# Kernel optimization log

Hardware: AMD Instinct MI355X
Metric: run time of the kernel (lower is better)

Reference implementation:

```python
import jax, jax.numpy as jnp
import numpy as np

N_NODES = 8192
N_FEAT = 256
N_EDGES = 131072
K = 4


def setup_inputs() -> dict:
    key = jax.random.key(0)
    k1, k2, k3 = jax.random.split(key, 3)
    x = jax.random.normal(k1, (N_NODES, N_FEAT), dtype=jnp.float32)
    edge_index = jax.random.randint(k2, (2, N_EDGES), 0, N_NODES, dtype=jnp.int64)
    edge_weight = jax.random.uniform(k3, (N_EDGES,), dtype=jnp.float32)
    return {"k": K, "x": x, "edge_index": edge_index, "edge_weight": edge_weight}


def reference(k, x, edge_index, edge_weight):
    n = x.shape[0]
    src, dst = edge_index[0], edge_index[1]
    # Symmetrized dense adjacency, matching the torch loop:
    #   adj[src, dst] = w  then  adj[dst, src] += w
    adj = jnp.zeros((n, n), dtype=x.dtype)
    adj = adj.at[src, dst].set(edge_weight)
    adj = adj.at[dst, src].add(edge_weight)
    # M = [I | A | A^2 | ... | A^{k-1}] (N x kN) times block_diag(x,...,x)
    # (kN x kF) is exactly concat([A^j @ x for j in 0..k-1], axis=1) -- we
    # compute that directly and never form the block-diagonal zeros.
    outs = [x]
    h = x
    for _ in range(1, k):
        h = adj @ h  # A^j @ x  (A symmetric, so order is immaterial)
        outs.append(h)
    return jnp.concatenate(outs, axis=1)  # [N, k*F]
```

## Files before the change

kernel.cpp:

```cpp
#include <hip/hip_runtime.h>

#define N_NODES 8192
#define N_FEAT  256
#define N_EDGES 131072
#define KPOW    4
#define OUT_LD  1024
#define RCAP    128
#define COL_MASK 8191u

typedef float    f32x4 __attribute__((ext_vector_type(4)));
typedef unsigned u32x4 __attribute__((ext_vector_type(4)));
typedef unsigned u32x2 __attribute__((ext_vector_type(2)));

static __device__ __forceinline__ float bflo(unsigned u) {
    union { unsigned i; float f; } v; v.i = u << 16; return v.f;
}
static __device__ __forceinline__ float bfhi(unsigned u) {
    union { unsigned i; float f; } v; v.i = u & 0xffff0000u; return v.f;
}
static __device__ __forceinline__ unsigned short f2bf(float f) {
    union { float f; unsigned i; } v = { f };
    return (unsigned short)((v.i + 0x7fffu + ((v.i >> 16) & 1u)) >> 16);
}

__global__ void k_scatter_copy(const int* __restrict__ ei, const float* __restrict__ ew,
                               int* __restrict__ len, u32x2* __restrict__ ent,
                               const float* __restrict__ x, float* __restrict__ out,
                               unsigned short* __restrict__ xb) {
    if (blockIdx.x < 2048) {
        int t = blockIdx.x * blockDim.x + threadIdx.x;
        int row = t >> 6;
        int lane = t & 63;
        f32x4 v = __builtin_nontemporal_load((const f32x4*)(x + (size_t)row * N_FEAT + lane * 4));
        __builtin_nontemporal_store(v, (f32x4*)(out + (size_t)row * OUT_LD + lane * 4));
        u32x2 pb;
        pb.x = ((unsigned)f2bf(v.y) << 16) | f2bf(v.x);
        pb.y = ((unsigned)f2bf(v.w) << 16) | f2bf(v.z);
        *(u32x2*)(xb + (size_t)row * N_FEAT + lane * 4) = pb;
    } else {
        int e = (blockIdx.x - 2048) * blockDim.x + threadIdx.x;
        if (e >= N_EDGES) return;
        int src = __builtin_nontemporal_load(ei + e);
        int dst = __builtin_nontemporal_load(ei + N_EDGES + e);
        unsigned wbits = __float_as_uint(__builtin_nontemporal_load(ew + e));
        int s0 = atomicAdd(&len[dst], 1);
        if (s0 < RCAP) {
            u32x2 v; v.x = (unsigned)src; v.y = wbits;
            ent[(size_t)dst * RCAP + s0] = v;
        }
        int s1 = atomicAdd(&len[src], 1);
        if (s1 < RCAP) {
            u32x2 v; v.x = (1u << 30) | ((unsigned)e << 13) | (unsigned)dst; v.y = wbits;
            ent[(size_t)src * RCAP + s1] = v;
        }
    }
}

__global__ __launch_bounds__(256) void k_spmm(const int* __restrict__ len,
                                              const u32x2* ent,
                                              unsigned* entw,
                                              const unsigned short* __restrict__ hinb,
                                              float* __restrict__ hout,
                                              unsigned short* __restrict__ houtb,
                                              int write_bf, int dedup) {
    __shared__ u32x2 sent[4 * RCAP];
    int wave = threadIdx.x >> 6;
    int lane = threadIdx.x & 63;
    int row = blockIdx.x * 4 + wave;
    int n = __builtin_amdgcn_readfirstlane(len[row]);
    if (n > RCAP) n = RCAP;

    const u32x2* ep = ent + (size_t)row * RCAP;
    u32x2* sp = sent + wave * RCAP;
    u32x2 e0 = __builtin_nontemporal_load(ep + lane);
    u32x2 e1 = __builtin_nontemporal_load(ep + 64 + lane);
    if (lane >= n)      e0.y = 0u;
    if (lane + 64 >= n) e1.y = 0u;

    if (dedup) {
        unsigned v0 = e0.x, v1 = e1.x;
        bool k0 = false, k1 = false;
        int j0 = n < 64 ? n : 64;
        for (int j = 0; j < j0; ++j) {
            unsigned b = (unsigned)__shfl((int)v0, j);
            if (b >> 30) {
                k0 |= (((b ^ v0) & COL_MASK) == 0u) && (b > v0);
                k1 |= (((b ^ v1) & COL_MASK) == 0u) && (b > v1);
            }
        }
        for (int j = 0; j < n - 64; ++j) {
            unsigned b = (unsigned)__shfl((int)v1, j);
            if (b >> 30) {
                k0 |= (((b ^ v0) & COL_MASK) == 0u) && (b > v0);
                k1 |= (((b ^ v1) & COL_MASK) == 0u) && (b > v1);
            }
        }
        size_t wbase = (size_t)row * RCAP * 2;
        if (lane < n && k0 && (v0 >> 30)) {
            e0.y = 0u; entw[wbase + 2 * lane + 1] = 0u;
        }
        int s1 = lane + 64;
        if (s1 < n && k1 && (v1 >> 30)) {
            e1.y = 0u; entw[wbase + 2 * s1 + 1] = 0u;
        }
    }

    sp[lane] = e0;
    sp[lane + 64] = e1;
    __builtin_amdgcn_s_waitcnt(0);

    int half = lane >> 5;
    int fl   = lane & 31;
    const unsigned short* hbase = hinb + fl * 8;
    float a0 = 0.f, a1 = 0.f, a2 = 0.f, a3 = 0.f,
          a4 = 0.f, a5 = 0.f, a6 = 0.f, a7 = 0.f;
    int ng = (n + 15) >> 4;

    for (int g = 0; g < ng; ++g) {
        const u32x2* ge = sp + g * 16 + half;
        u32x4 us[8];
#pragma unroll
        for (int t = 0; t < 8; ++t) {
            unsigned c = ge[2 * t].x & COL_MASK;
            us[t] = *(const u32x4*)(hbase + (size_t)c * N_FEAT);
        }
#pragma unroll
        for (int t = 0; t < 8; ++t) {
            float w = __uint_as_float(ge[2 * t].y);
            a0 += w * bflo(us[t].x); a1 += w * bfhi(us[t].x);
            a2 += w * bflo(us[t].y); a3 += w * bfhi(us[t].y);
            a4 += w * bflo(us[t].z); a5 += w * bfhi(us[t].z);
            a6 += w * bflo(us[t].w); a7 += w * bfhi(us[t].w);
        }
    }

    a0 += __shfl_xor(a0, 32); a1 += __shfl_xor(a1, 32);
    a2 += __shfl_xor(a2, 32); a3 += __shfl_xor(a3, 32);
    a4 += __shfl_xor(a4, 32); a5 += __shfl_xor(a5, 32);
    a6 += __shfl_xor(a6, 32); a7 += __shfl_xor(a7, 32);

    if (half == 0) {
        float* op = hout + (size_t)row * OUT_LD + fl * 8;
        f32x4 r0; r0.x = a0; r0.y = a1; r0.z = a2; r0.w = a3;
        f32x4 r1; r1.x = a4; r1.y = a5; r1.z = a6; r1.w = a7;
        __builtin_nontemporal_store(r0, (f32x4*)op);
        __builtin_nontemporal_store(r1, (f32x4*)(op + 4));
    } else if (write_bf) {
        u32x4 pb;
        pb.x = ((unsigned)f2bf(a1) << 16) | f2bf(a0);
        pb.y = ((unsigned)f2bf(a3) << 16) | f2bf(a2);
        pb.z = ((unsigned)f2bf(a5) << 16) | f2bf(a4);
        pb.w = ((unsigned)f2bf(a7) << 16) | f2bf(a6);
        *(u32x4*)(houtb + (size_t)row * N_FEAT + fl * 8) = pb;
    }
}

extern "C" void kernel_launch(void* const* d_in, const int* in_sizes, int n_in,
                              void* d_out, int out_size, void* d_ws, size_t ws_size,
                              hipStream_t stream) {
    const float* x  = (const float*)d_in[1];
    const int*   ei = (const int*)d_in[2];
    const float* ew = (const float*)d_in[3];
    float* out = (float*)d_out;

    int* len   = (int*)d_ws;
    u32x2* ent = (u32x2*)(len + N_NODES);
    unsigned short* hb0 = (unsigned short*)(ent + (size_t)N_NODES * RCAP);
    unsigned short* hb1 = hb0 + (size_t)N_NODES * N_FEAT;
    unsigned short* hb2 = hb1 + (size_t)N_NODES * N_FEAT;

    (void)hipMemsetAsync(len, 0, (size_t)N_NODES * sizeof(int), stream);

    const int TB = 256;
    const int EB = N_EDGES / TB;

    k_scatter_copy<<<2048 + EB, TB, 0, stream>>>(ei, ew, len, ent, x, out, hb0);

    const unsigned short* hin = hb0;
    for (int j = 1; j < KPOW; ++j) {
        float* hout = out + (size_t)j * N_FEAT;
        unsigned short* houtb = (j == 1) ? hb1 : hb2;
        int write_bf = (j < KPOW - 1) ? 1 : 0;
        int dedup    = (j == 1) ? 1 : 0;
        k_spmm<<<N_NODES / 4, TB, 0, stream>>>(len, ent, (unsigned*)ent, hin,
                                               hout, houtb, write_bf, dedup);
        hin = houtb;
    }
}
```

Before: 134.9 us.

## Gather fp32 features directly from output instead of bf16 side buffers

Drops the bf16 copies of the feature matrices. Each SpMM pass now gathers fp32 rows straight from x or from the previous output slice (stride 1024), with one lane per 4 features, 8 neighbours per group and no cross-half reduction. This removes the bf16 conversion and pack work and the extra side-buffer writes. In exchange each gather moves twice as many bytes, and the input rows sit in the strided output that stays cache-resident through regular stores. The second entry load and its LDS store are also skipped when a row has 64 or fewer entries.

```diff
diff --git a/kernel.cpp b/kernel.cpp
--- a/kernel.cpp
+++ b/kernel.cpp
@@ -9,37 +9,19 @@
 #define COL_MASK 8191u
 
 typedef float    f32x4 __attribute__((ext_vector_type(4)));
-typedef unsigned u32x4 __attribute__((ext_vector_type(4)));
 typedef unsigned u32x2 __attribute__((ext_vector_type(2)));
-
-static __device__ __forceinline__ float bflo(unsigned u) {
-    union { unsigned i; float f; } v; v.i = u << 16; return v.f;
-}
-static __device__ __forceinline__ float bfhi(unsigned u) {
-    union { unsigned i; float f; } v; v.i = u & 0xffff0000u; return v.f;
-}
-static __device__ __forceinline__ unsigned short f2bf(float f) {
-    union { float f; unsigned i; } v = { f };
-    return (unsigned short)((v.i + 0x7fffu + ((v.i >> 16) & 1u)) >> 16);
-}
 
 __global__ void k_scatter_copy(const int* __restrict__ ei, const float* __restrict__ ew,
                                int* __restrict__ len, u32x2* __restrict__ ent,
-                               const float* __restrict__ x, float* __restrict__ out,
-                               unsigned short* __restrict__ xb) {
+                               const float* __restrict__ x, float* __restrict__ out) {
     if (blockIdx.x < 2048) {
         int t = blockIdx.x * blockDim.x + threadIdx.x;
         int row = t >> 6;
         int lane = t & 63;
-        f32x4 v = __builtin_nontemporal_load((const f32x4*)(x + (size_t)row * N_FEAT + lane * 4));
+        f32x4 v = *(const f32x4*)(x + (size_t)row * N_FEAT + lane * 4);
         __builtin_nontemporal_store(v, (f32x4*)(out + (size_t)row * OUT_LD + lane * 4));
-        u32x2 pb;
-        pb.x = ((unsigned)f2bf(v.y) << 16) | f2bf(v.x);
-        pb.y = ((unsigned)f2bf(v.w) << 16) | f2bf(v.z);
-        *(u32x2*)(xb + (size_t)row * N_FEAT + lane * 4) = pb;
     } else {
         int e = (blockIdx.x - 2048) * blockDim.x + threadIdx.x;
-        if (e >= N_EDGES) return;
         int src = __builtin_nontemporal_load(ei + e);
         int dst = __builtin_nontemporal_load(ei + N_EDGES + e);
         unsigned wbits = __float_as_uint(__builtin_nontemporal_load(ew + e));
@@ -59,10 +41,10 @@
 __global__ __launch_bounds__(256) void k_spmm(const int* __restrict__ len,
                                               const u32x2* ent,
                                               unsigned* entw,
-                                              const unsigned short* __restrict__ hinb,
+                                              const float* __restrict__ hin,
+                                              int hstride,
                                               float* __restrict__ hout,
-                                              unsigned short* __restrict__ houtb,
-                                              int write_bf, int dedup) {
+                                              int nt_out, int dedup) {
     __shared__ u32x2 sent[4 * RCAP];
     int wave = threadIdx.x >> 6;
     int lane = threadIdx.x & 63;
@@ -72,10 +54,14 @@
 
     const u32x2* ep = ent + (size_t)row * RCAP;
     u32x2* sp = sent + wave * RCAP;
-    u32x2 e0 = __builtin_nontemporal_load(ep + lane);
-    u32x2 e1 = __builtin_nontemporal_load(ep + 64 + lane);
-    if (lane >= n)      e0.y = 0u;
-    if (lane + 64 >= n) e1.y = 0u;
+    u32x2 e0 = ep[lane];
+    if (lane >= n) e0.y = 0u;
+    u32x2 e1; e1.x = 0u; e1.y = 0u;
+    bool two = (n > 64);
+    if (two) {
+        e1 = ep[64 + lane];
+        if (lane + 64 >= n) e1.y = 0u;
+    }
 
     if (dedup) {
         unsigned v0 = e0.x, v1 = e1.x;
@@ -100,59 +86,42 @@
             e0.y = 0u; entw[wbase + 2 * lane + 1] = 0u;
         }
         int s1 = lane + 64;
-        if (s1 < n && k1 && (v1 >> 30)) {
+        if (two && s1 < n && k1 && (v1 >> 30)) {
             e1.y = 0u; entw[wbase + 2 * s1 + 1] = 0u;
         }
     }
 
     sp[lane] = e0;
-    sp[lane + 64] = e1;
+    if (two) sp[lane + 64] = e1;
     __builtin_amdgcn_s_waitcnt(0);
 
-    int half = lane >> 5;
-    int fl   = lane & 31;
-    const unsigned short* hbase = hinb + fl * 8;
-    float a0 = 0.f, a1 = 0.f, a2 = 0.f, a3 = 0.f,
-          a4 = 0.f, a5 = 0.f, a6 = 0.f, a7 = 0.f;
-    int ng = (n + 15) >> 4;
+    const float* hbase = hin + lane * 4;
+    float a0 = 0.f, a1 = 0.f, a2 = 0.f, a3 = 0.f;
+    int ng = (n + 7) >> 3;
 
     for (int g = 0; g < ng; ++g) {
-        const u32x2* ge = sp + g * 16 + half;
-        u32x4 us[8];
+        const u32x2* ge = sp + g * 8;
+        u32x2 cw[8];
+        f32x4 us[8];
+#pragma unroll
+        for (int t = 0; t < 8; ++t) cw[t] = ge[t];
 #pragma unroll
         for (int t = 0; t < 8; ++t) {
-            unsigned c = ge[2 * t].x & COL_MASK;
-            us[t] = *(const u32x4*)(hbase + (size_t)c * N_FEAT);
+            unsigned c = cw[t].x & COL_MASK;
+            us[t] = *(const f32x4*)(hbase + (size_t)c * hstride);
         }
 #pragma unroll
         for (int t = 0; t < 8; ++t) {
-            float w = __uint_as_float(ge[2 * t].y);
-            a0 += w * bflo(us[t].x); a1 += w * bfhi(us[t].x);
-            a2 += w * bflo(us[t].y); a3 += w * bfhi(us[t].y);
-            a4 += w * bflo(us[t].z); a5 += w * bfhi(us[t].z);
-            a6 += w * bflo(us[t].w); a7 += w * bfhi(us[t].w);
+            float w = __uint_as_float(cw[t].y);
+            a0 += w * us[t].x; a1 += w * us[t].y;
+            a2 += w * us[t].z; a3 += w * us[t].w;
         }
     }
 
-    a0 += __shfl_xor(a0, 32); a1 += __shfl_xor(a1, 32);
-    a2 += __shfl_xor(a2, 32); a3 += __shfl_xor(a3, 32);
-    a4 += __shfl_xor(a4, 32); a5 += __shfl_xor(a5, 32);
-    a6 += __shfl_xor(a6, 32); a7 += __shfl_xor(a7, 32);
-
-    if (half == 0) {
-        float* op = hout + (size_t)row * OUT_LD + fl * 8;
-        f32x4 r0; r0.x = a0; r0.y = a1; r0.z = a2; r0.w = a3;
-        f32x4 r1; r1.x = a4; r1.y = a5; r1.z = a6; r1.w = a7;
-        __builtin_nontemporal_store(r0, (f32x4*)op);
-        __builtin_nontemporal_store(r1, (f32x4*)(op + 4));
-    } else if (write_bf) {
-        u32x4 pb;
-        pb.x = ((unsigned)f2bf(a1) << 16) | f2bf(a0);
-        pb.y = ((unsigned)f2bf(a3) << 16) | f2bf(a2);
-        pb.z = ((unsigned)f2bf(a5) << 16) | f2bf(a4);
-        pb.w = ((unsigned)f2bf(a7) << 16) | f2bf(a6);
-        *(u32x4*)(houtb + (size_t)row * N_FEAT + fl * 8) = pb;
-    }
+    f32x4 r; r.x = a0; r.y = a1; r.z = a2; r.w = a3;
+    f32x4* op = (f32x4*)(hout + (size_t)row * OUT_LD + lane * 4);
+    if (nt_out) __builtin_nontemporal_store(r, op);
+    else        *op = r;
 }
 
 extern "C" void kernel_launch(void* const* d_in, const int* in_sizes, int n_in,
@@ -165,25 +134,21 @@
 
     int* len   = (int*)d_ws;
     u32x2* ent = (u32x2*)(len + N_NODES);
-    unsigned short* hb0 = (unsigned short*)(ent + (size_t)N_NODES * RCAP);
-    unsigned short* hb1 = hb0 + (size_t)N_NODES * N_FEAT;
-    unsigned short* hb2 = hb1 + (size_t)N_NODES * N_FEAT;
 
     (void)hipMemsetAsync(len, 0, (size_t)N_NODES * sizeof(int), stream);
 
     const int TB = 256;
     const int EB = N_EDGES / TB;
 
-    k_scatter_copy<<<2048 + EB, TB, 0, stream>>>(ei, ew, len, ent, x, out, hb0);
+    k_scatter_copy<<<2048 + EB, TB, 0, stream>>>(ei, ew, len, ent, x, out);
 
-    const unsigned short* hin = hb0;
     for (int j = 1; j < KPOW; ++j) {
-        float* hout = out + (size_t)j * N_FEAT;
-        unsigned short* houtb = (j == 1) ? hb1 : hb2;
-        int write_bf = (j < KPOW - 1) ? 1 : 0;
-        int dedup    = (j == 1) ? 1 : 0;
-        k_spmm<<<N_NODES / 4, TB, 0, stream>>>(len, ent, (unsigned*)ent, hin,
-                                               hout, houtb, write_bf, dedup);
-        hin = houtb;
+        const float* hin = (j == 1) ? x : (out + (size_t)(j - 1) * N_FEAT);
+        int hstride      = (j == 1) ? N_FEAT : OUT_LD;
+        float* hout      = out + (size_t)j * N_FEAT;
+        int nt_out       = (j == KPOW - 1) ? 1 : 0;
+        int dedup        = (j == 1) ? 1 : 0;
+        k_spmm<<<N_NODES / 4, TB, 0, stream>>>(len, ent, (unsigned*)ent,
+                                               hin, hstride, hout, nt_out, dedup);
     }
 }
```

After: 165.5 us. 22.7% more time.
